# Optimization experiments

Measured on AMD Instinct MI355X. Metric: run time of the kernel, lower is better.

Reference implementation:

```python
import jax, jax.numpy as jnp
import numpy as np
import math

B, L, LC = 2, 2048, 2048
D_MODEL, D_CROSS, D_HEAD = 1024, 1024, 64
N_HEADS = D_MODEL // D_HEAD
D6 = D_HEAD // 6  # freq bands per spatial axis (k-diffusion AxialRoPE, 3 axes)
EPS = 1e-6


def rope_freqs():
    n = N_HEADS * D6
    f = jnp.exp(jnp.linspace(math.log(math.pi), math.log(10.0 * math.pi), n + 1)[:-1])
    return f.reshape(D6, N_HEADS).T  # [nh, d6]


def rope_theta(pos):
    # pos: [b, l, 3] -> theta: [b, nh, l, 3*d6]
    f = rope_freqs()
    th = jnp.concatenate([pos[..., None, a:a + 1] * f for a in range(3)], axis=-1)  # [b,l,nh,3*d6]
    return jnp.moveaxis(th, -2, -3)


def apply_rotary(x, theta):
    d = theta.shape[-1]
    x1, x2, x3 = x[..., :d], x[..., d:2 * d], x[..., 2 * d:]
    c, s = jnp.cos(theta), jnp.sin(theta)
    return jnp.concatenate([x1 * c - x2 * s, x2 * c + x1 * s, x3], axis=-1)


def rms_norm(x, scale, eps=EPS):
    ms = jnp.mean(x * x, axis=-1, keepdims=True)
    return x * (scale * jax.lax.rsqrt(ms + eps))


def cosine_scale(q, k, scale, eps=EPS):
    s = jnp.sqrt(scale)[:, None, None]  # [nh,1,1]
    qn = q * (s * jax.lax.rsqrt(jnp.sum(q * q, axis=-1, keepdims=True) + eps))
    kn = k * (s * jax.lax.rsqrt(jnp.sum(k * k, axis=-1, keepdims=True) + eps))
    return qn, kn


def setup_inputs():
    key = jax.random.key(0)
    ks = jax.random.split(key, 8)
    return {
        "x": jax.random.normal(ks[0], (B, L, D_MODEL), jnp.float32),
        "pos": jax.random.uniform(ks[1], (B, L, 3), jnp.float32),
        "x_cross": jax.random.normal(ks[2], (B, LC, D_CROSS), jnp.float32),
        "pos_cross": jax.random.uniform(ks[3], (B, LC, 3), jnp.float32),
        "norm_scale": jnp.ones((D_MODEL,), jnp.float32),
        "norm_cross_scale": jnp.ones((D_CROSS,), jnp.float32),
        "q_w": jax.random.normal(ks[4], (D_MODEL, D_MODEL), jnp.float32) * 0.02,
        "kv_w": jax.random.normal(ks[5], (2 * D_MODEL, D_CROSS), jnp.float32) * 0.02,
        "head_scale": jnp.full((N_HEADS,), 10.0, jnp.float32),
        "out_w": jax.random.normal(ks[6], (D_MODEL, D_MODEL), jnp.float32) * 0.02,
    }


def reference(x, pos, x_cross, pos_cross, norm_scale, norm_cross_scale, q_w, kv_w, head_scale, out_w):
    skip = x
    xn = rms_norm(x, norm_scale)
    xc = rms_norm(x_cross, norm_cross_scale)
    q = xn @ q_w.T                       # [b,l,d]
    kv = xc @ kv_w.T                     # [b,lc,2d]
    b, l, _ = q.shape
    lc = kv.shape[1]
    q = q.reshape(b, l, N_HEADS, D_HEAD).transpose(0, 2, 1, 3)          # [b,nh,l,e]
    kv = kv.reshape(b, lc, 2, N_HEADS, D_HEAD)                          # (t nh e) factorization
    k = kv[:, :, 0].transpose(0, 2, 1, 3)
    v = kv[:, :, 1].transpose(0, 2, 1, 3)
    q, k = cosine_scale(q, k, head_scale)
    q = apply_rotary(q, rope_theta(pos))
    k = apply_rotary(k, rope_theta(pos_cross))
    attn = jax.nn.softmax(jnp.einsum('bhqe,bhke->bhqk', q, k), axis=-1)  # scale=1.0 (cosine-sim pre-scaled)
    o = jnp.einsum('bhqk,bhke->bhqe', attn, v)
    o = o.transpose(0, 2, 1, 3).reshape(b, l, D_MODEL)
    return o @ out_w.T + skip
```

## Files before the change

kernel.cpp:

```cpp
#include <hip/hip_runtime.h>

typedef __bf16 bf16_t;
typedef __bf16 bf16x4 __attribute__((ext_vector_type(4)));
typedef __bf16 bf16x8 __attribute__((ext_vector_type(8)));
typedef float f32x4 __attribute__((ext_vector_type(4)));

#define B_DIM 2
#define L_DIM 2048
#define LC_DIM 2048
#define DM 1024
#define NH 16
#define DH 64
#define MB (1u << 20)

__device__ __forceinline__ bool probe_is_f32(const unsigned* probe) {
  return probe[0] == 0x3F800000u;
}

__device__ __forceinline__ void async16(const bf16_t* g, bf16_t* l) {
  __builtin_amdgcn_global_load_lds((const __attribute__((address_space(1))) void*)g,
                                   (__attribute__((address_space(3))) void*)l, 16, 0, 0);
}

__global__ __launch_bounds__(256) void conv_bf16_k(const void* __restrict__ src,
                                                   bf16_t* __restrict__ dst, int n,
                                                   const unsigned* __restrict__ probe) {
  const int i = (blockIdx.x * 256 + threadIdx.x) * 4;
  if (i >= n) return;
  bf16x4 w;
  if (probe_is_f32(probe)) {
    f32x4 v = *(const f32x4*)((const float*)src + i);
    w[0] = (bf16_t)v[0]; w[1] = (bf16_t)v[1]; w[2] = (bf16_t)v[2]; w[3] = (bf16_t)v[3];
  } else {
    w = *(const bf16x4*)((const bf16_t*)src + i);
  }
  *(bf16x4*)(dst + i) = w;
}

__global__ __launch_bounds__(256) void conv_f32_k(const void* __restrict__ src,
                                                  float* __restrict__ dst, int n,
                                                  const unsigned* __restrict__ probe) {
  const int i = (blockIdx.x * 256 + threadIdx.x) * 4;
  if (i >= n) return;
  f32x4 v;
  if (probe_is_f32(probe)) {
    v = *(const f32x4*)((const float*)src + i);
  } else {
    bf16x4 w = *(const bf16x4*)((const bf16_t*)src + i);
    v[0] = (float)w[0]; v[1] = (float)w[1]; v[2] = (float)w[2]; v[3] = (float)w[3];
  }
  *(f32x4*)(dst + i) = v;
}

__global__ __launch_bounds__(256) void norm_cast_k(const void* __restrict__ src,
                                                   const float* __restrict__ scale,
                                                   bf16_t* __restrict__ out,
                                                   const unsigned* __restrict__ probe) {
  const int row = blockIdx.x;
  const int tid = threadIdx.x;
  float f0, f1, f2, f3;
  if (probe_is_f32(probe)) {
    f32x4 v = *((const f32x4*)((const float*)src + (size_t)row * DM) + tid);
    f0 = v[0]; f1 = v[1]; f2 = v[2]; f3 = v[3];
  } else {
    bf16x4 v = *((const bf16x4*)((const bf16_t*)src + (size_t)row * DM) + tid);
    f0 = (float)v[0]; f1 = (float)v[1]; f2 = (float)v[2]; f3 = (float)v[3];
  }
  float ss = f0 * f0 + f1 * f1 + f2 * f2 + f3 * f3;
#pragma unroll
  for (int m = 1; m < 64; m <<= 1) ss += __shfl_xor(ss, m, 64);
  __shared__ float red[4];
  const int wave = tid >> 6, lane = tid & 63;
  if (lane == 0) red[wave] = ss;
  __syncthreads();
  float ms = (red[0] + red[1] + red[2] + red[3]) * (1.0f / DM);
  float r = rsqrtf(ms + 1e-6f);
  f32x4 sc = *(const f32x4*)(scale + tid * 4);
  bf16x4 w;
  w[0] = (bf16_t)(f0 * r * sc[0]);
  w[1] = (bf16_t)(f1 * r * sc[1]);
  w[2] = (bf16_t)(f2 * r * sc[2]);
  w[3] = (bf16_t)(f3 * r * sc[3]);
  *(bf16x4*)(out + (size_t)row * DM + tid * 4) = w;
}

__global__ __launch_bounds__(256) void gemm_qkv_k(const bf16_t* __restrict__ xn,
                                                  const bf16_t* __restrict__ xcn,
                                                  const bf16_t* __restrict__ qw,
                                                  const bf16_t* __restrict__ kvw,
                                                  bf16_t* __restrict__ qb,
                                                  bf16_t* __restrict__ kvK,
                                                  bf16_t* __restrict__ VtO) {
  __shared__ bf16_t Asm[128 * 32];
  __shared__ bf16_t Wsm[128 * 32];
  const int tid = threadIdx.x;
  const int wave = tid >> 6, lane = tid & 63;
  const int quad = lane >> 4, tc = lane & 15;
  const int wr = wave >> 1, wc = wave & 1;
  const bool isq = blockIdx.y < 8;
  const bf16_t* A = isq ? xn : xcn;
  const bf16_t* W = isq ? qw : kvw;
  const int n0 = (isq ? blockIdx.y : (blockIdx.y - 8)) * 128;
  const int m0 = blockIdx.x * 128;
  const int K = 1024;

  const int srow = wave * 16 + (lane >> 2);
  const int scol = (lane & 3) * 8;
  const bf16_t* ag = A + (size_t)(m0 + srow) * K + scol;
  const bf16_t* wg = W + (size_t)(n0 + srow) * K + scol;
  bf16_t* al0 = &Asm[(wave * 16) * 32];
  bf16_t* al1 = &Asm[(64 + wave * 16) * 32];
  bf16_t* wl0 = &Wsm[(wave * 16) * 32];
  bf16_t* wl1 = &Wsm[(64 + wave * 16) * 32];

  f32x4 acc[4][4] = {};

  for (int k0 = 0; k0 < K; k0 += 32) {
    async16(ag + k0, al0);
    async16(ag + k0 + (size_t)64 * K, al1);
    async16(wg + k0, wl0);
    async16(wg + k0 + (size_t)64 * K, wl1);
    __syncthreads();
    bf16x8 af[4], wf[4];
#pragma unroll
    for (int i = 0; i < 4; ++i)
      af[i] = *(const bf16x8*)&Asm[(wr * 64 + i * 16 + tc) * 32 + quad * 8];
#pragma unroll
    for (int j = 0; j < 4; ++j)
      wf[j] = *(const bf16x8*)&Wsm[(wc * 64 + j * 16 + tc) * 32 + quad * 8];
#pragma unroll
    for (int i = 0; i < 4; ++i)
#pragma unroll
      for (int j = 0; j < 4; ++j)
        acc[i][j] = __builtin_amdgcn_mfma_f32_16x16x32_bf16(af[i], wf[j], acc[i][j], 0, 0, 0);
    __syncthreads();
  }

  if (isq || n0 < DM) {
    bf16_t* C = isq ? qb : kvK;
#pragma unroll
    for (int i = 0; i < 4; ++i) {
      const size_t row = (size_t)m0 + wr * 64 + i * 16 + quad * 4;
#pragma unroll
      for (int j = 0; j < 4; ++j) {
        const int col = n0 + wc * 64 + j * 16 + tc;
#pragma unroll
        for (int r = 0; r < 4; ++r)
          C[(row + r) * DM + col] = (bf16_t)acc[i][j][r];
      }
    }
  } else {
#pragma unroll
    for (int i = 0; i < 4; ++i) {
      const int row = m0 + wr * 64 + i * 16 + quad * 4;
      const int b = row >> 11, kc = row & (LC_DIM - 1);
#pragma unroll
      for (int j = 0; j < 4; ++j) {
        const int hd = n0 - DM + wc * 64 + j * 16 + tc;
        bf16x4 pk;
        pk[0] = (bf16_t)acc[i][j][0];
        pk[1] = (bf16_t)acc[i][j][1];
        pk[2] = (bf16_t)acc[i][j][2];
        pk[3] = (bf16_t)acc[i][j][3];
        *(bf16x4*)(VtO + ((size_t)b * NH * DH + hd) * LC_DIM + kc) = pk;
      }
    }
  }
}

__global__ __launch_bounds__(256) void prep_k(bf16_t* __restrict__ q,
                                              const bf16_t* __restrict__ kvK,
                                              bf16_t* __restrict__ Kp,
                                              const float* __restrict__ pos,
                                              const float* __restrict__ pos_cross,
                                              const float* __restrict__ head_scale) {
  const int gw = (blockIdx.x * blockDim.x + threadIdx.x) >> 6;
  const int lane = threadIdx.x & 63;
  const int per = B_DIM * L_DIM * NH;
  const bool is_k = gw >= per;
  const int id = is_k ? gw - per : gw;
  const int h = id & 15;
  const int row = id >> 4;
  const bf16_t* src = (is_k ? kvK : q) + (size_t)row * DM + h * DH;
  const float* pp = (is_k ? pos_cross : pos) + (size_t)row * 3;

  float val = (float)src[lane];
  float ss = val * val;
#pragma unroll
  for (int m = 1; m < 64; m <<= 1) ss += __shfl_xor(ss, m, 64);
  float sc = sqrtf(head_scale[h]) * rsqrtf(ss + 1e-6f);
  float vn = val * sc;

  const int j = lane;
  const int tj = j < 30 ? j : (j < 60 ? j - 30 : 0);
  const int a = tj >= 20 ? 2 : (tj >= 10 ? 1 : 0);
  const int jj = tj - a * 10;
  float p = pp[a];
  float freq = 3.14159265358979f * expf((float)(jj * 16 + h) * 0.014391156831f);
  float th = p * freq;
  float cth = cosf(th), sth = sinf(th);
  const int partner = j < 30 ? j + 30 : (j < 60 ? j - 30 : j);
  float vp = __shfl(vn, partner, 64);
  float outv;
  if (j < 30)       outv = vn * cth - vp * sth;
  else if (j < 60)  outv = vn * cth + vp * sth;
  else              outv = vn;

  if (is_k) {
    const int b = row >> 11, l = row & (LC_DIM - 1);
    Kp[(((size_t)b * NH + h) * LC_DIM + l) * DH + lane] = (bf16_t)outv;
  } else {
    q[(size_t)row * DM + h * DH + lane] = (bf16_t)outv;
  }
}

__global__ __launch_bounds__(128, 2) void flash3_k(const bf16_t* __restrict__ q,
                                                   const bf16_t* __restrict__ Kp,
                                                   const bf16_t* __restrict__ Vt,
                                                   const float* __restrict__ head_scale,
                                                   bf16_t* __restrict__ Op,
                                                   float* __restrict__ lp) {
  __shared__ bf16_t Ksm[64 * 64];
  __shared__ bf16_t Vsm[64 * 64];
  __shared__ bf16_t Psm[2 * 64 * 64];

  const int tid = threadIdx.x;
  const int wave = tid >> 6, lane = tid & 63;
  const int quad = lane >> 4, tc = lane & 15;
  const int bh = blockIdx.y, b = bh >> 4, h = bh & 15;
  const int z = blockIdx.z;
  const int q0 = blockIdx.x * 128 + wave * 64;
  const float M = head_scale[h];
  const int sw = tc & 7;

  bf16x8 qf[4][2];
#pragma unroll
  for (int jj = 0; jj < 4; ++jj)
#pragma unroll
    for (int hf = 0; hf < 2; ++hf)
      qf[jj][hf] = *(const bf16x8*)(q + (size_t)(b * L_DIM + q0 + jj * 16 + tc) * DM +
                                    h * DH + hf * 32 + quad * 8);

  f32x4 accO[4][4] = {};
  float lsum[4] = {0.f, 0.f, 0.f, 0.f};

  const bf16_t* kg = Kp + (size_t)bh * LC_DIM * DH;
  const bf16_t* vg = Vt + (size_t)bh * DH * LC_DIM;
  bf16_t* Pw = &Psm[wave * 64 * 64];

  const int trow = tid >> 3;
  const int tch = tid & 7;

  for (int kc0 = z * 1024; kc0 < z * 1024 + 1024; kc0 += 64) {
#pragma unroll
    for (int i = 0; i < 4; ++i) {
      const int row = trow + i * 16;
      const int pc = (tch ^ (row & 7)) * 8;
      *(bf16x8*)&Ksm[row * 64 + pc] = *(const bf16x8*)(kg + (size_t)(kc0 + row) * DH + tch * 8);
      *(bf16x8*)&Vsm[row * 64 + pc] = *(const bf16x8*)(vg + (size_t)row * LC_DIM + kc0 + tch * 8);
    }
    __syncthreads();

    bf16x8 kfr[4][2];
#pragma unroll
    for (int mt = 0; mt < 4; ++mt)
#pragma unroll
      for (int hf = 0; hf < 2; ++hf)
        kfr[mt][hf] = *(const bf16x8*)&Ksm[(mt * 16 + tc) * 64 + ((hf * 4 + quad) ^ sw) * 8];

#pragma unroll
    for (int jj = 0; jj < 4; ++jj) {
      f32x4 s[4];
#pragma unroll
      for (int mt = 0; mt < 4; ++mt) {
        f32x4 zf = {0.f, 0.f, 0.f, 0.f};
        zf = __builtin_amdgcn_mfma_f32_16x16x32_bf16(kfr[mt][0], qf[jj][0], zf, 0, 0, 0);
        zf = __builtin_amdgcn_mfma_f32_16x16x32_bf16(kfr[mt][1], qf[jj][1], zf, 0, 0, 0);
        s[mt] = zf;
      }
#pragma unroll
      for (int mt = 0; mt < 4; ++mt) {
        float p0 = __expf(s[mt][0] - M);
        float p1 = __expf(s[mt][1] - M);
        float p2 = __expf(s[mt][2] - M);
        float p3 = __expf(s[mt][3] - M);
        lsum[jj] += (p0 + p1) + (p2 + p3);
        bf16x4 pk;
        pk[0] = (bf16_t)p0; pk[1] = (bf16_t)p1; pk[2] = (bf16_t)p2; pk[3] = (bf16_t)p3;
        const int phys = (mt * 2 + (quad >> 1)) ^ sw;
        *(bf16x4*)&Pw[(jj * 16 + tc) * 64 + phys * 8 + (quad & 1) * 4] = pk;
      }
    }

#pragma unroll
    for (int kb = 0; kb < 2; ++kb) {
      bf16x8 vf[4];
#pragma unroll
      for (int dt = 0; dt < 4; ++dt)
        vf[dt] = *(const bf16x8*)&Vsm[(dt * 16 + tc) * 64 + ((kb * 4 + quad) ^ sw) * 8];
#pragma unroll
      for (int jp = 0; jp < 4; ++jp) {
        bf16x8 pf = *(const bf16x8*)&Pw[(jp * 16 + tc) * 64 + ((kb * 4 + quad) ^ sw) * 8];
#pragma unroll
        for (int dt = 0; dt < 4; ++dt)
          accO[jp][dt] = __builtin_amdgcn_mfma_f32_16x16x32_bf16(pf, vf[dt], accO[jp][dt], 0, 0, 0);
      }
    }
    __syncthreads();
  }

#pragma unroll
  for (int jj = 0; jj < 4; ++jj) {
    lsum[jj] += __shfl_xor(lsum[jj], 16, 64);
    lsum[jj] += __shfl_xor(lsum[jj], 32, 64);
  }
  bf16_t* Ob = Op + (size_t)(z * 32 + bh) * L_DIM * DH;
  float* lb = lp + (size_t)(z * 32 + bh) * L_DIM;
#pragma unroll
  for (int jj = 0; jj < 4; ++jj) {
    if (quad == 0) lb[q0 + jj * 16 + tc] = lsum[jj];
#pragma unroll
    for (int r = 0; r < 4; ++r) {
      const size_t qg = q0 + jj * 16 + quad * 4 + r;
#pragma unroll
      for (int dt = 0; dt < 4; ++dt)
        Ob[qg * DH + dt * 16 + tc] = (bf16_t)accO[jj][dt][r];
    }
  }
}

__global__ __launch_bounds__(256) void combine_k(const bf16_t* __restrict__ Op,
                                                 const float* __restrict__ lp,
                                                 bf16_t* __restrict__ ob) {
  const size_t t = (size_t)blockIdx.x * 256 + threadIdx.x;
  const int bh = (int)(t >> 15);
  const int rem = (int)(t & 32767);
  const int l = rem >> 4, d4 = (rem & 15) * 4;
  const size_t base = ((size_t)bh * L_DIM + l) * DH + d4;
  const size_t zoff = (size_t)32 * L_DIM * DH;
  bf16x4 a0 = *(const bf16x4*)(Op + base);
  bf16x4 a1 = *(const bf16x4*)(Op + zoff + base);
  const float linv = 1.f / (lp[(size_t)bh * L_DIM + l] + lp[(size_t)32 * L_DIM + bh * L_DIM + l]);
  bf16x4 w;
#pragma unroll
  for (int e = 0; e < 4; ++e) w[e] = (bf16_t)(((float)a0[e] + (float)a1[e]) * linv);
  const int b = bh >> 4, h = bh & 15;
  *(bf16x4*)(ob + ((size_t)(b * L_DIM + l)) * DM + h * DH + d4) = w;
}

__global__ __launch_bounds__(256) void gemm_out_k(const bf16_t* __restrict__ A,
                                                  const bf16_t* __restrict__ W,
                                                  const void* __restrict__ skip_raw,
                                                  void* __restrict__ out,
                                                  const unsigned* __restrict__ probe) {
  __shared__ bf16_t Asm[64 * 32];
  __shared__ bf16_t Wsm[128 * 32];
  const int tid = threadIdx.x;
  const int wave = tid >> 6, lane = tid & 63;
  const int quad = lane >> 4, tc = lane & 15;
  const int wr = wave >> 1, wc = wave & 1;
  const int m0 = blockIdx.x * 64, n0 = blockIdx.y * 128;
  const int K = 1024, N = 1024;

  const int srow = wave * 16 + (lane >> 2);
  const int scol = (lane & 3) * 8;
  const bf16_t* ag = A + (size_t)(m0 + srow) * K + scol;
  const bf16_t* wg = W + (size_t)(n0 + srow) * K + scol;
  bf16_t* al = &Asm[(wave * 16) * 32];
  bf16_t* wl0 = &Wsm[(wave * 16) * 32];
  bf16_t* wl1 = &Wsm[(64 + wave * 16) * 32];

  f32x4 acc[2][4] = {};

  for (int k0 = 0; k0 < K; k0 += 32) {
    async16(ag + k0, al);
    async16(wg + k0, wl0);
    async16(wg + k0 + (size_t)64 * K, wl1);
    __syncthreads();
    bf16x8 af[2], wf[4];
#pragma unroll
    for (int i = 0; i < 2; ++i)
      af[i] = *(const bf16x8*)&Asm[(wr * 32 + i * 16 + tc) * 32 + quad * 8];
#pragma unroll
    for (int j = 0; j < 4; ++j)
      wf[j] = *(const bf16x8*)&Wsm[(wc * 64 + j * 16 + tc) * 32 + quad * 8];
#pragma unroll
    for (int i = 0; i < 2; ++i)
#pragma unroll
      for (int j = 0; j < 4; ++j)
        acc[i][j] = __builtin_amdgcn_mfma_f32_16x16x32_bf16(af[i], wf[j], acc[i][j], 0, 0, 0);
    __syncthreads();
  }

  const bool f32o = probe_is_f32(probe);
#pragma unroll
  for (int i = 0; i < 2; ++i) {
    const size_t row = (size_t)m0 + wr * 32 + i * 16 + quad * 4;
#pragma unroll
    for (int j = 0; j < 4; ++j) {
      const int col = n0 + wc * 64 + j * 16 + tc;
#pragma unroll
      for (int r = 0; r < 4; ++r) {
        const size_t idx = (row + r) * (size_t)N + col;
        float v = acc[i][j][r];
        if (f32o) {
          v += ((const float*)skip_raw)[idx];
          ((float*)out)[idx] = v;
        } else {
          v += (float)((const bf16_t*)skip_raw)[idx];
          ((bf16_t*)out)[idx] = (bf16_t)v;
        }
      }
    }
  }
}

extern "C" void kernel_launch(void* const* d_in, const int* in_sizes, int n_in,
                              void* d_out, int out_size, void* d_ws, size_t ws_size,
                              hipStream_t stream) {
  const unsigned* probe = (const unsigned*)d_in[4];
  char* ws = (char*)d_ws;

  bf16_t* cow  = (bf16_t*)(ws + 0 * MB);
  bf16_t* cqw  = (bf16_t*)(ws + 2 * MB);
  bf16_t* ckvw = (bf16_t*)(ws + 4 * MB);
  bf16_t* xn   = (bf16_t*)(ws + 8 * MB);
  bf16_t* xcn  = (bf16_t*)(ws + 16 * MB);
  bf16_t* Op   = (bf16_t*)(ws + 8 * MB);
  bf16_t* kvK  = (bf16_t*)(ws + 24 * MB);
  bf16_t* qb   = (bf16_t*)(ws + 32 * MB);
  bf16_t* Vt   = (bf16_t*)(ws + 40 * MB);
  bf16_t* Kp   = (bf16_t*)(ws + 48 * MB);
  bf16_t* ob   = (bf16_t*)(ws + 56 * MB);
  float* lp    = (float*)(ws + 64 * MB);
  float* fpos  = (float*)(ws + 65 * MB);
  float* fposc = (float*)(ws + 65 * MB + 64 * 1024);
  float* fns   = (float*)(ws + 65 * MB + 128 * 1024);
  float* fncs  = (float*)(ws + 65 * MB + 144 * 1024);
  float* fhs   = (float*)(ws + 65 * MB + 160 * 1024);

  conv_bf16_k<<<(DM * DM) / 1024, 256, 0, stream>>>(d_in[6], cqw, DM * DM, probe);
  conv_bf16_k<<<(2 * DM * DM) / 1024, 256, 0, stream>>>(d_in[7], ckvw, 2 * DM * DM, probe);
  conv_bf16_k<<<(DM * DM) / 1024, 256, 0, stream>>>(d_in[9], cow, DM * DM, probe);
  conv_f32_k<<<12, 256, 0, stream>>>(d_in[1], fpos, B_DIM * L_DIM * 3, probe);
  conv_f32_k<<<12, 256, 0, stream>>>(d_in[3], fposc, B_DIM * LC_DIM * 3, probe);
  conv_f32_k<<<1, 256, 0, stream>>>(d_in[4], fns, DM, probe);
  conv_f32_k<<<1, 256, 0, stream>>>(d_in[5], fncs, DM, probe);
  conv_f32_k<<<1, 256, 0, stream>>>(d_in[8], fhs, NH, probe);

  norm_cast_k<<<B_DIM * L_DIM, 256, 0, stream>>>(d_in[0], fns, xn, probe);
  norm_cast_k<<<B_DIM * LC_DIM, 256, 0, stream>>>(d_in[2], fncs, xcn, probe);
  gemm_qkv_k<<<dim3(32, 24), 256, 0, stream>>>(xn, xcn, cqw, ckvw, qb, kvK, Vt);
  prep_k<<<(2 * B_DIM * L_DIM * NH) / 4, 256, 0, stream>>>(qb, kvK, Kp, fpos, fposc, fhs);
  flash3_k<<<dim3(L_DIM / 128, B_DIM * NH, 2), 128, 0, stream>>>(qb, Kp, Vt, fhs, Op, lp);
  combine_k<<<4096, 256, 0, stream>>>(Op, lp, ob);
  gemm_out_k<<<dim3(64, 8), 256, 0, stream>>>(ob, cow, d_in[0], d_out, probe);
}
```

Measured before the change: 270.8 us.

## Merge conversion and norm launches, use exp2 softmax, single-wave flash without LDS staging

The eight small conversion launches become one kernel, and the two RMS-norm launches become one, cutting launch overhead. Q is pre-scaled by log2(e) so the softmax can use the hardware exp2 instruction. The flash kernel becomes a single-wave block that loads K and V fragments straight from global memory into registers, dropping shared-memory staging and barriers. In exchange, K/V reuse across waves is lost, so global and L2 traffic per query tile rises and each load is exposed without double buffering.

```diff
diff --git a/kernel.cpp b/kernel.cpp
--- a/kernel.cpp
+++ b/kernel.cpp
@@ -12,6 +12,7 @@
 #define NH 16
 #define DH 64
 #define MB (1u << 20)
+#define LOG2E 1.44269504088896f
 
 __device__ __forceinline__ bool probe_is_f32(const unsigned* probe) {
   return probe[0] == 0x3F800000u;
@@ -22,13 +23,9 @@
                                    (__attribute__((address_space(3))) void*)l, 16, 0, 0);
 }
 
-__global__ __launch_bounds__(256) void conv_bf16_k(const void* __restrict__ src,
-                                                   bf16_t* __restrict__ dst, int n,
-                                                   const unsigned* __restrict__ probe) {
-  const int i = (blockIdx.x * 256 + threadIdx.x) * 4;
-  if (i >= n) return;
+__device__ __forceinline__ void conv_b(const void* src, bf16_t* dst, int i, bool f32) {
   bf16x4 w;
-  if (probe_is_f32(probe)) {
+  if (f32) {
     f32x4 v = *(const f32x4*)((const float*)src + i);
     w[0] = (bf16_t)v[0]; w[1] = (bf16_t)v[1]; w[2] = (bf16_t)v[2]; w[3] = (bf16_t)v[3];
   } else {
@@ -36,14 +33,10 @@
   }
   *(bf16x4*)(dst + i) = w;
 }
-
-__global__ __launch_bounds__(256) void conv_f32_k(const void* __restrict__ src,
-                                                  float* __restrict__ dst, int n,
-                                                  const unsigned* __restrict__ probe) {
-  const int i = (blockIdx.x * 256 + threadIdx.x) * 4;
+__device__ __forceinline__ void conv_f(const void* src, float* dst, int i, int n, bool f32) {
   if (i >= n) return;
   f32x4 v;
-  if (probe_is_f32(probe)) {
+  if (f32) {
     v = *(const f32x4*)((const float*)src + i);
   } else {
     bf16x4 w = *(const bf16x4*)((const bf16_t*)src + i);
@@ -52,11 +45,36 @@
   *(f32x4*)(dst + i) = v;
 }
 
-__global__ __launch_bounds__(256) void norm_cast_k(const void* __restrict__ src,
-                                                   const float* __restrict__ scale,
-                                                   bf16_t* __restrict__ out,
+__global__ __launch_bounds__(256) void conv_all_k(
+    const void* qw, const void* kvw, const void* ow, const void* pos,
+    const void* posc, const void* ns, const void* ncs, const void* hs,
+    bf16_t* cqw, bf16_t* ckvw, bf16_t* cow, float* fpos, float* fposc,
+    float* fns, float* fncs, float* fhs, const unsigned* probe) {
+  const bool f32 = probe_is_f32(probe);
+  const int blk = blockIdx.x;
+  const int e4 = threadIdx.x * 4;
+  if (blk < 1024)       conv_b(qw,  cqw,  blk * 1024 + e4, f32);
+  else if (blk < 3072)  conv_b(kvw, ckvw, (blk - 1024) * 1024 + e4, f32);
+  else if (blk < 4096)  conv_b(ow,  cow,  (blk - 3072) * 1024 + e4, f32);
+  else if (blk < 4108)  conv_f(pos,  fpos,  (blk - 4096) * 1024 + e4, 12288, f32);
+  else if (blk < 4120)  conv_f(posc, fposc, (blk - 4108) * 1024 + e4, 12288, f32);
+  else if (blk == 4120) conv_f(ns,  fns,  e4, 1024, f32);
+  else if (blk == 4121) conv_f(ncs, fncs, e4, 1024, f32);
+  else                  conv_f(hs,  fhs,  e4, 16, f32);
+}
+
+__global__ __launch_bounds__(256) void norm_both_k(const void* __restrict__ srcA,
+                                                   const void* __restrict__ srcB,
+                                                   const float* __restrict__ scA,
+                                                   const float* __restrict__ scB,
+                                                   bf16_t* __restrict__ outA,
+                                                   bf16_t* __restrict__ outB,
                                                    const unsigned* __restrict__ probe) {
-  const int row = blockIdx.x;
+  const bool isB = blockIdx.x >= B_DIM * L_DIM;
+  const int row = isB ? blockIdx.x - B_DIM * L_DIM : blockIdx.x;
+  const void* src = isB ? srcB : srcA;
+  const float* scale = isB ? scB : scA;
+  bf16_t* out = isB ? outB : outA;
   const int tid = threadIdx.x;
   float f0, f1, f2, f3;
   if (probe_is_f32(probe)) {
@@ -189,6 +207,7 @@
 #pragma unroll
   for (int m = 1; m < 64; m <<= 1) ss += __shfl_xor(ss, m, 64);
   float sc = sqrtf(head_scale[h]) * rsqrtf(ss + 1e-6f);
+  if (!is_k) sc *= LOG2E;
   float vn = val * sc;
 
   const int j = lane;
@@ -214,23 +233,20 @@
   }
 }
 
-__global__ __launch_bounds__(128, 2) void flash3_k(const bf16_t* __restrict__ q,
-                                                   const bf16_t* __restrict__ Kp,
-                                                   const bf16_t* __restrict__ Vt,
-                                                   const float* __restrict__ head_scale,
-                                                   bf16_t* __restrict__ Op,
-                                                   float* __restrict__ lp) {
-  __shared__ bf16_t Ksm[64 * 64];
-  __shared__ bf16_t Vsm[64 * 64];
-  __shared__ bf16_t Psm[2 * 64 * 64];
-
-  const int tid = threadIdx.x;
-  const int wave = tid >> 6, lane = tid & 63;
+__global__ __launch_bounds__(64) void flash4_k(const bf16_t* __restrict__ q,
+                                               const bf16_t* __restrict__ Kp,
+                                               const bf16_t* __restrict__ Vt,
+                                               const float* __restrict__ head_scale,
+                                               bf16_t* __restrict__ Op,
+                                               float* __restrict__ lp) {
+  __shared__ bf16_t Psm[64 * 64];
+
+  const int lane = threadIdx.x;
   const int quad = lane >> 4, tc = lane & 15;
   const int bh = blockIdx.y, b = bh >> 4, h = bh & 15;
   const int z = blockIdx.z;
-  const int q0 = blockIdx.x * 128 + wave * 64;
-  const float M = head_scale[h];
+  const int q0 = blockIdx.x * 64;
+  const float M2 = head_scale[h] * LOG2E;
   const int sw = tc & 7;
 
   bf16x8 qf[4][2];
@@ -246,27 +262,15 @@
 
   const bf16_t* kg = Kp + (size_t)bh * LC_DIM * DH;
   const bf16_t* vg = Vt + (size_t)bh * DH * LC_DIM;
-  bf16_t* Pw = &Psm[wave * 64 * 64];
-
-  const int trow = tid >> 3;
-  const int tch = tid & 7;
 
   for (int kc0 = z * 1024; kc0 < z * 1024 + 1024; kc0 += 64) {
-#pragma unroll
-    for (int i = 0; i < 4; ++i) {
-      const int row = trow + i * 16;
-      const int pc = (tch ^ (row & 7)) * 8;
-      *(bf16x8*)&Ksm[row * 64 + pc] = *(const bf16x8*)(kg + (size_t)(kc0 + row) * DH + tch * 8);
-      *(bf16x8*)&Vsm[row * 64 + pc] = *(const bf16x8*)(vg + (size_t)row * LC_DIM + kc0 + tch * 8);
-    }
-    __syncthreads();
-
     bf16x8 kfr[4][2];
 #pragma unroll
     for (int mt = 0; mt < 4; ++mt)
 #pragma unroll
       for (int hf = 0; hf < 2; ++hf)
-        kfr[mt][hf] = *(const bf16x8*)&Ksm[(mt * 16 + tc) * 64 + ((hf * 4 + quad) ^ sw) * 8];
+        kfr[mt][hf] = *(const bf16x8*)(kg + (size_t)(kc0 + mt * 16 + tc) * DH +
+                                       hf * 32 + quad * 8);
 
 #pragma unroll
     for (int jj = 0; jj < 4; ++jj) {
@@ -280,15 +284,15 @@
       }
 #pragma unroll
       for (int mt = 0; mt < 4; ++mt) {
-        float p0 = __expf(s[mt][0] - M);
-        float p1 = __expf(s[mt][1] - M);
-        float p2 = __expf(s[mt][2] - M);
-        float p3 = __expf(s[mt][3] - M);
+        float p0 = __builtin_amdgcn_exp2f(s[mt][0] - M2);
+        float p1 = __builtin_amdgcn_exp2f(s[mt][1] - M2);
+        float p2 = __builtin_amdgcn_exp2f(s[mt][2] - M2);
+        float p3 = __builtin_amdgcn_exp2f(s[mt][3] - M2);
         lsum[jj] += (p0 + p1) + (p2 + p3);
         bf16x4 pk;
         pk[0] = (bf16_t)p0; pk[1] = (bf16_t)p1; pk[2] = (bf16_t)p2; pk[3] = (bf16_t)p3;
         const int phys = (mt * 2 + (quad >> 1)) ^ sw;
-        *(bf16x4*)&Pw[(jj * 16 + tc) * 64 + phys * 8 + (quad & 1) * 4] = pk;
+        *(bf16x4*)&Psm[(jj * 16 + tc) * 64 + phys * 8 + (quad & 1) * 4] = pk;
       }
     }
 
@@ -297,16 +301,16 @@
       bf16x8 vf[4];
 #pragma unroll
       for (int dt = 0; dt < 4; ++dt)
-        vf[dt] = *(const bf16x8*)&Vsm[(dt * 16 + tc) * 64 + ((kb * 4 + quad) ^ sw) * 8];
+        vf[dt] = *(const bf16x8*)(vg + (size_t)(dt * 16 + tc) * LC_DIM +
+                                  kc0 + kb * 32 + quad * 8);
 #pragma unroll
       for (int jp = 0; jp < 4; ++jp) {
-        bf16x8 pf = *(const bf16x8*)&Pw[(jp * 16 + tc) * 64 + ((kb * 4 + quad) ^ sw) * 8];
+        bf16x8 pf = *(const bf16x8*)&Psm[(jp * 16 + tc) * 64 + ((kb * 4 + quad) ^ sw) * 8];
 #pragma unroll
         for (int dt = 0; dt < 4; ++dt)
           accO[jp][dt] = __builtin_amdgcn_mfma_f32_16x16x32_bf16(pf, vf[dt], accO[jp][dt], 0, 0, 0);
       }
     }
-    __syncthreads();
   }
 
 #pragma unroll
@@ -439,20 +443,14 @@
   float* fncs  = (float*)(ws + 65 * MB + 144 * 1024);
   float* fhs   = (float*)(ws + 65 * MB + 160 * 1024);
 
-  conv_bf16_k<<<(DM * DM) / 1024, 256, 0, stream>>>(d_in[6], cqw, DM * DM, probe);
-  conv_bf16_k<<<(2 * DM * DM) / 1024, 256, 0, stream>>>(d_in[7], ckvw, 2 * DM * DM, probe);
-  conv_bf16_k<<<(DM * DM) / 1024, 256, 0, stream>>>(d_in[9], cow, DM * DM, probe);
-  conv_f32_k<<<12, 256, 0, stream>>>(d_in[1], fpos, B_DIM * L_DIM * 3, probe);
-  conv_f32_k<<<12, 256, 0, stream>>>(d_in[3], fposc, B_DIM * LC_DIM * 3, probe);
-  conv_f32_k<<<1, 256, 0, stream>>>(d_in[4], fns, DM, probe);
-  conv_f32_k<<<1, 256, 0, stream>>>(d_in[5], fncs, DM, probe);
-  conv_f32_k<<<1, 256, 0, stream>>>(d_in[8], fhs, NH, probe);
-
-  norm_cast_k<<<B_DIM * L_DIM, 256, 0, stream>>>(d_in[0], fns, xn, probe);
-  norm_cast_k<<<B_DIM * LC_DIM, 256, 0, stream>>>(d_in[2], fncs, xcn, probe);
+  conv_all_k<<<4123, 256, 0, stream>>>(d_in[6], d_in[7], d_in[9], d_in[1], d_in[3],
+                                       d_in[4], d_in[5], d_in[8],
+                                       cqw, ckvw, cow, fpos, fposc, fns, fncs, fhs, probe);
+  norm_both_k<<<2 * B_DIM * L_DIM, 256, 0, stream>>>(d_in[0], d_in[2], fns, fncs,
+                                                     xn, xcn, probe);
   gemm_qkv_k<<<dim3(32, 24), 256, 0, stream>>>(xn, xcn, cqw, ckvw, qb, kvK, Vt);
   prep_k<<<(2 * B_DIM * L_DIM * NH) / 4, 256, 0, stream>>>(qb, kvK, Kp, fpos, fposc, fhs);
-  flash3_k<<<dim3(L_DIM / 128, B_DIM * NH, 2), 128, 0, stream>>>(qb, Kp, Vt, fhs, Op, lp);
+  flash4_k<<<dim3(L_DIM / 64, B_DIM * NH, 2), 64, 0, stream>>>(qb, Kp, Vt, fhs, Op, lp);
   combine_k<<<4096, 256, 0, stream>>>(Op, lp, ob);
   gemm_out_k<<<dim3(64, 8), 256, 0, stream>>>(ob, cow, d_in[0], d_out, probe);
 }
```

Result: no change. 269.7 us (-0.4%).
